# Kernel optimization log

Hardware: AMD Instinct MI355X
Metric: run time of the kernel (lower is better)

## Reference

```python
import jax, jax.numpy as jnp
import numpy as np

D_MODEL = 1024
N_HEADS = 16


def setup_inputs() -> dict:
    key = jax.random.key(0)
    ks = jax.random.split(key, 11)
    B, S = 4, 2048
    sc = 1.0 / np.sqrt(D_MODEL)
    inp = {
        "Q": jax.random.normal(ks[0], (B, S, D_MODEL), jnp.float32),
        "K": jax.random.normal(ks[1], (B, S, D_MODEL), jnp.float32),
        "V": jax.random.normal(ks[2], (B, S, D_MODEL), jnp.float32),
        "Wq": jax.random.normal(ks[3], (D_MODEL, D_MODEL), jnp.float32) * sc,
        "bq": jnp.zeros((D_MODEL,), jnp.float32),
        "Wk": jax.random.normal(ks[4], (D_MODEL, D_MODEL), jnp.float32) * sc,
        "bk": jnp.zeros((D_MODEL,), jnp.float32),
        "Wv": jax.random.normal(ks[5], (D_MODEL, D_MODEL), jnp.float32) * sc,
        "bv": jnp.zeros((D_MODEL,), jnp.float32),
        "Wo": jax.random.normal(ks[6], (D_MODEL, D_MODEL), jnp.float32) * sc,
        "bo": jnp.zeros((D_MODEL,), jnp.float32),
    }
    return inp


def reference(Q, K, V, Wq, bq, Wk, bk, Wv, bv, Wo, bo):
    B, Sq, d_model = Q.shape
    h = N_HEADS
    d_k = d_model // h

    def split_heads(x, W, b):
        y = x @ W.T + b                     # (B, S, d_model)
        return y.reshape(B, x.shape[1], h, d_k).transpose(0, 2, 1, 3)  # (B,h,S,d_k)

    q = split_heads(Q, Wq, bq)
    k = split_heads(K, Wk, bk)
    v = split_heads(V, Wv, bv)

    scores = jnp.einsum("bhqd,bhkd->bhqk", q, k) / jnp.sqrt(jnp.asarray(d_k, q.dtype))
    attn = jax.nn.softmax(scores.astype(jnp.float32), axis=-1).astype(q.dtype)
    out = jnp.einsum("bhqk,bhkd->bhqd", attn, v)  # (B,h,Sq,d_k)
    out = out.transpose(0, 2, 1, 3).reshape(B, Sq, d_model)
    return out @ Wo.T + bo
```

## Files before the change

kernel.cpp:

```cpp
#include <hip/hip_runtime.h>
#include <stdint.h>

#define DM    1024
#define NH    16
#define DKH   64
#define SEQ   2048
#define NB    4
#define MROWS (NB * SEQ)

typedef __attribute__((ext_vector_type(4))) float f32x4;
typedef __attribute__((ext_vector_type(8))) short s16x8;
typedef __attribute__((ext_vector_type(4))) unsigned short u16x4;
typedef __attribute__((ext_vector_type(8))) unsigned short u16x8;

__device__ __forceinline__ unsigned short f2bf(float f) {
  union { float f; uint32_t u; } v; v.f = f;
  uint32_t r = v.u + 0x7fffu + ((v.u >> 16) & 1u);
  return (unsigned short)(r >> 16);
}

__device__ __forceinline__ void gload16(const void* g, void* l) {
  __builtin_amdgcn_global_load_lds(
      (__attribute__((address_space(1))) void*)(uintptr_t)g,
      (__attribute__((address_space(3))) void*)(uint32_t)(uintptr_t)l,
      16, 0, 0);
}

__device__ __forceinline__ float exp2fast(float x) {
#if __has_builtin(__builtin_amdgcn_exp2f)
  return __builtin_amdgcn_exp2f(x);
#else
  return exp2f(x);
#endif
}

__device__ __forceinline__ unsigned int cvtpk(float a, float b) {
  unsigned int r;
  asm("v_cvt_pk_bf16_f32 %0, %1, %2" : "=v"(r) : "v"(a), "v"(b));
  return r;
}

__device__ __forceinline__ float bperm(float v, int srclane) {
  union { float f; int i; } u; u.f = v;
  u.i = __builtin_amdgcn_ds_bpermute(srclane << 2, u.i);
  return u.f;
}

__device__ __forceinline__ void cvt8(const float* in, unsigned short* out, int i) {
  const f32x4* p = (const f32x4*)(in + i);
  f32x4 a = p[0], b = p[1];
  u16x8 r;
#pragma unroll
  for (int j = 0; j < 4; ++j) { r[j] = f2bf(a[j]); r[4 + j] = f2bf(b[j]); }
  *(u16x8*)(out + i) = r;
}

__global__ __launch_bounds__(256) void cvt3_kernel(const float* __restrict__ a,
                                                   const float* __restrict__ b,
                                                   const float* __restrict__ c,
                                                   unsigned short* __restrict__ oa,
                                                   unsigned short* __restrict__ ob,
                                                   unsigned short* __restrict__ oc) {
  const int seg = blockIdx.x >> 12;
  const int blk = blockIdx.x & 4095;
  const float* in = (seg == 0) ? a : (seg == 1) ? b : c;
  unsigned short* out = (seg == 0) ? oa : (seg == 1) ? ob : oc;
  cvt8(in, out, (blk * 256 + threadIdx.x) * 8);
}

__global__ __launch_bounds__(256) void cvt4_kernel(const float* __restrict__ a,
                                                   const float* __restrict__ b,
                                                   const float* __restrict__ c,
                                                   const float* __restrict__ d,
                                                   unsigned short* __restrict__ oa,
                                                   unsigned short* __restrict__ ob,
                                                   unsigned short* __restrict__ oc,
                                                   unsigned short* __restrict__ od) {
  const int seg = blockIdx.x >> 9;
  const int blk = blockIdx.x & 511;
  const float* in = (seg == 0) ? a : (seg == 1) ? b : (seg == 2) ? c : d;
  unsigned short* out = (seg == 0) ? oa : (seg == 1) ? ob : (seg == 2) ? oc : od;
  cvt8(in, out, (blk * 256 + threadIdx.x) * 8);
}

template <int MODE>
__global__ __launch_bounds__(256) void gemm_bt(const unsigned short* __restrict__ A,
                                               const unsigned short* __restrict__ Bw,
                                               const float* __restrict__ bias,
                                               void* __restrict__ out,
                                               float oscale) {
  __shared__ char smem[65536];

  int bid = (int)(blockIdx.y * 8 + blockIdx.x);
  bid = (bid & 7) * 64 + (bid >> 3);
  const int tcol = (bid & 7) * 128;
  const int trow = (bid >> 3) * 128;

  const int lane = threadIdx.x & 63;
  const int w    = threadIdx.x >> 6;
  const int wm = w >> 1, wn = w & 1;
  const int l15 = lane & 15, l4 = lane >> 4;

  f32x4 acc[4][4] = {};

  auto stage = [&](int buf, int k0) {
    char* As = smem + buf * 32768;
    char* Bs = As + 16384;
#pragma unroll
    for (int i = 0; i < 4; ++i) {
      const int row = i * 32 + w * 8 + (lane >> 3);
      const int sc  = ((lane & 7) ^ (row & 7)) << 3;
      gload16(A  + (size_t)(trow + row) * DM + k0 + sc, As + i * 4096 + w * 1024);
      gload16(Bw + (size_t)(tcol + row) * DM + k0 + sc, Bs + i * 4096 + w * 1024);
    }
  };

  stage(0, 0);
  __syncthreads();
  int cur = 0;

  for (int k0 = 0; k0 < DM; k0 += 64) {
    if (k0 + 64 < DM) stage(cur ^ 1, k0 + 64);
    char* As = smem + cur * 32768;
    char* Bs = As + 16384;

#pragma unroll
    for (int ks = 0; ks < 2; ++ks) {
      s16x8 af[4], bf[4];
#pragma unroll
      for (int x = 0; x < 4; ++x) {
        const int ra = wm * 64 + x * 16 + l15;
        const int rb = wn * 64 + x * 16 + l15;
        const int kb = ks * 4 + l4;
        af[x] = *(const s16x8*)(As + ra * 128 + ((kb ^ (ra & 7)) << 4));
        bf[x] = *(const s16x8*)(Bs + rb * 128 + ((kb ^ (rb & 7)) << 4));
      }
#pragma unroll
      for (int mi = 0; mi < 4; ++mi)
#pragma unroll
        for (int ni = 0; ni < 4; ++ni)
          acc[mi][ni] = __builtin_amdgcn_mfma_f32_16x16x32_bf16(af[mi], bf[ni], acc[mi][ni], 0, 0, 0);
    }
    __syncthreads();
    cur ^= 1;
  }

#pragma unroll
  for (int ni = 0; ni < 4; ++ni) {
    const int n  = tcol + wn * 64 + ni * 16 + l15;
    const float bv = bias[n];
#pragma unroll
    for (int mi = 0; mi < 4; ++mi) {
      const int m0 = trow + wm * 64 + mi * 16 + l4 * 4;
      if (MODE == 2) {
        float* o = (float*)out;
#pragma unroll
        for (int j = 0; j < 4; ++j)
          o[(size_t)(m0 + j) * DM + n] = acc[mi][ni][j] + bv;
      } else if (MODE == 0) {
        unsigned short* o = (unsigned short*)out;
        const int bb = m0 >> 11, h = n >> 6, dk = n & 63;
#pragma unroll
        for (int j = 0; j < 4; ++j) {
          const int s = (m0 + j) & 2047;
          o[(((size_t)bb * NH + h) * SEQ + s) * DKH + dk] = f2bf((acc[mi][ni][j] + bv) * oscale);
        }
      } else {
        unsigned short* o = (unsigned short*)out;
        const int bb = m0 >> 11, h = n >> 6, dk = n & 63, s = m0 & 2047;
        const int u = s & 31;
        const int s2 = (s & ~31) | ((u & 12) << 1) | ((u & 16) >> 2);
        u16x4 pk;
#pragma unroll
        for (int j = 0; j < 4; ++j) pk[j] = f2bf(acc[mi][ni][j] + bv);
        *(u16x4*)(o + (((size_t)bb * NH + h) * DKH + dk) * SEQ + s2) = pk;
      }
    }
  }
}

__global__ __launch_bounds__(256, 2) void attn_kernel(const unsigned short* __restrict__ qh,
                                                      const unsigned short* __restrict__ kh,
                                                      const unsigned short* __restrict__ vth,
                                                      unsigned short* __restrict__ ao) {
  __shared__ char smem[32768];

  int bid = (int)blockIdx.x;
  bid = (bid & 7) * 64 + (bid >> 3);
  const int bh = bid >> 3;
  const int q0 = (bid & 7) * 256;

  const int lane = threadIdx.x & 63;
  const int w    = threadIdx.x >> 6;
  const int l15 = lane & 15, l4 = lane >> 4;

  const int qrow = q0 + w * 64;
  const unsigned short* qbase = qh + ((size_t)bh * SEQ + qrow) * DKH;

  s16x8 qf[4][2];
#pragma unroll
  for (int ni = 0; ni < 4; ++ni)
#pragma unroll
    for (int ks = 0; ks < 2; ++ks)
      qf[ni][ks] = *(const s16x8*)(qbase + (ni * 16 + l15) * DKH + ks * 32 + l4 * 8);

  int koff[2][4], voff[2][4];
#pragma unroll
  for (int ks = 0; ks < 2; ++ks)
#pragma unroll
    for (int mi = 0; mi < 4; ++mi) {
      const int r = mi * 16 + l15;
      koff[ks][mi] = r * 128 + (((ks * 4 + l4) ^ (r & 7)) << 4);
    }
#pragma unroll
  for (int m = 0; m < 2; ++m)
#pragma unroll
    for (int nd = 0; nd < 4; ++nd) {
      const int r = nd * 16 + l15;
      voff[m][nd] = r * 128 + (((m * 4 + l4) ^ (r & 7)) << 4);
    }

  f32x4 o[4][4] = {};
  f32x4 lsum[4] = {};

  s16x8 onesB = (s16x8)0;
  if (l15 == 0) {
#pragma unroll
    for (int j = 0; j < 8; ++j) onesB[j] = (short)0x3F80;
  }

  const unsigned short* kbase = kh  + (size_t)bh * SEQ * DKH;
  const unsigned short* vbase = vth + (size_t)bh * DKH * SEQ;

  auto stageK = [&](int buf, int kv0) {
    char* Ks = smem + buf * 8192;
#pragma unroll
    for (int i = 0; i < 2; ++i) {
      const int row = i * 32 + w * 8 + (lane >> 3);
      const int sc  = ((lane & 7) ^ (row & 7)) << 3;
      gload16(kbase + (size_t)(kv0 + row) * DKH + sc, Ks + i * 4096 + w * 1024);
    }
  };
  auto stageV = [&](int buf, int kv0) {
    char* Vs = smem + 16384 + buf * 8192;
#pragma unroll
    for (int i = 0; i < 2; ++i) {
      const int row = i * 32 + w * 8 + (lane >> 3);
      const int sc  = ((lane & 7) ^ (row & 7)) << 3;
      gload16(vbase + (size_t)row * SEQ + kv0 + sc, Vs + i * 4096 + w * 1024);
    }
  };

  f32x4 sa[4][4];

  auto qkt = [&](const char* Ks) {
#pragma unroll
    for (int mi = 0; mi < 4; ++mi)
#pragma unroll
      for (int ni = 0; ni < 4; ++ni) sa[mi][ni] = (f32x4)0.f;
    __builtin_amdgcn_s_setprio(1);
#pragma unroll
    for (int ks = 0; ks < 2; ++ks) {
      s16x8 kf[4];
#pragma unroll
      for (int mi = 0; mi < 4; ++mi) kf[mi] = *(const s16x8*)(Ks + koff[ks][mi]);
#pragma unroll
      for (int mi = 0; mi < 4; ++mi)
#pragma unroll
        for (int ni = 0; ni < 4; ++ni)
          sa[mi][ni] = __builtin_amdgcn_mfma_f32_16x16x32_bf16(kf[mi], qf[ni][ks], sa[mi][ni], 0, 0, 0);
    }
    __builtin_amdgcn_s_setprio(0);
  };

  auto smpv = [&](const char* Vs) {
#pragma unroll
    for (int mi = 0; mi < 4; ++mi)
#pragma unroll
      for (int ni = 0; ni < 4; ++ni)
#pragma unroll
        for (int j = 0; j < 4; ++j)
          sa[mi][ni][j] = exp2fast(sa[mi][ni][j]);

    __builtin_amdgcn_s_setprio(1);
#pragma unroll
    for (int m = 0; m < 2; ++m) {
      s16x8 pa[4];
#pragma unroll
      for (int ni = 0; ni < 4; ++ni) {
        union { unsigned int u[4]; s16x8 v; } pu;
        pu.u[0] = cvtpk(sa[2 * m][ni][0],     sa[2 * m][ni][1]);
        pu.u[1] = cvtpk(sa[2 * m][ni][2],     sa[2 * m][ni][3]);
        pu.u[2] = cvtpk(sa[2 * m + 1][ni][0], sa[2 * m + 1][ni][1]);
        pu.u[3] = cvtpk(sa[2 * m + 1][ni][2], sa[2 * m + 1][ni][3]);
        pa[ni] = pu.v;
      }
#pragma unroll
      for (int ni = 0; ni < 4; ++ni)
        lsum[ni] = __builtin_amdgcn_mfma_f32_16x16x32_bf16(pa[ni], onesB, lsum[ni], 0, 0, 0);
#pragma unroll
      for (int nd = 0; nd < 4; ++nd) {
        const s16x8 vbf = *(const s16x8*)(Vs + voff[m][nd]);
#pragma unroll
        for (int ni = 0; ni < 4; ++ni)
          o[ni][nd] = __builtin_amdgcn_mfma_f32_16x16x32_bf16(pa[ni], vbf, o[ni][nd], 0, 0, 0);
      }
    }
    __builtin_amdgcn_s_setprio(0);
  };

  stageK(0, 0); stageV(0, 0);
  __syncthreads();

  for (int t = 0; t < 32; t += 2) {
    const int kv0 = t * 64;
    stageK(1, kv0 + 64); stageV(1, kv0 + 64);
    qkt(smem);
    smpv(smem + 16384);
    __syncthreads();
    if (t + 2 < 32) { stageK(0, kv0 + 128); stageV(0, kv0 + 128); }
    qkt(smem + 8192);
    smpv(smem + 16384 + 8192);
    __syncthreads();
  }

  const int bb = bh >> 4, h = bh & 15;
#pragma unroll
  for (int ni = 0; ni < 4; ++ni) {
#pragma unroll
    for (int j = 0; j < 4; ++j) {
      const float inv = 1.0f / bperm(lsum[ni][j], lane & 48);
      const int s = qrow + ni * 16 + l4 * 4 + j;
#pragma unroll
      for (int nd = 0; nd < 4; ++nd) {
        const int col = h * 64 + nd * 16 + l15;
        ao[((size_t)bb * SEQ + s) * DM + col] = f2bf(o[ni][nd][j] * inv);
      }
    }
  }
}

extern "C" void kernel_launch(void* const* d_in, const int* in_sizes, int n_in,
                              void* d_out, int out_size, void* d_ws, size_t ws_size,
                              hipStream_t stream) {
  const float* Q  = (const float*)d_in[0];
  const float* K  = (const float*)d_in[1];
  const float* V  = (const float*)d_in[2];
  const float* Wq = (const float*)d_in[3];
  const float* bq = (const float*)d_in[4];
  const float* Wk = (const float*)d_in[5];
  const float* bk = (const float*)d_in[6];
  const float* Wv = (const float*)d_in[7];
  const float* bv = (const float*)d_in[8];
  const float* Wo = (const float*)d_in[9];
  const float* bo = (const float*)d_in[10];
  float* out = (float*)d_out;

  char* ws = (char*)d_ws;
  const size_t MB = 1024 * 1024;
  unsigned short* Qb  = (unsigned short*)(ws + 0 * MB);
  unsigned short* Kb  = (unsigned short*)(ws + 16 * MB);
  unsigned short* Vb  = (unsigned short*)(ws + 32 * MB);
  unsigned short* Wqb = (unsigned short*)(ws + 48 * MB);
  unsigned short* Wkb = (unsigned short*)(ws + 50 * MB);
  unsigned short* Wvb = (unsigned short*)(ws + 52 * MB);
  unsigned short* Wob = (unsigned short*)(ws + 54 * MB);
  unsigned short* qhd = (unsigned short*)(ws + 56 * MB);
  unsigned short* khd = (unsigned short*)(ws + 72 * MB);
  unsigned short* vtd = (unsigned short*)(ws + 88 * MB);
  unsigned short* aod = (unsigned short*)(ws + 104 * MB);

  const float QSCALE = 0.18033688011112042f;

  cvt3_kernel<<<dim3(3 * 4096), 256, 0, stream>>>(Q, K, V, Qb, Kb, Vb);
  cvt4_kernel<<<dim3(4 * 512), 256, 0, stream>>>(Wq, Wk, Wv, Wo, Wqb, Wkb, Wvb, Wob);

  dim3 gg(DM / 128, MROWS / 128);
  gemm_bt<0><<<gg, 256, 0, stream>>>(Qb, Wqb, bq, qhd, QSCALE);
  gemm_bt<0><<<gg, 256, 0, stream>>>(Kb, Wkb, bk, khd, 1.0f);
  gemm_bt<1><<<gg, 256, 0, stream>>>(Vb, Wvb, bv, vtd, 1.0f);

  attn_kernel<<<dim3(512), 256, 0, stream>>>(qhd, khd, vtd, aod);

  gemm_bt<2><<<gg, 256, 0, stream>>>(aod, Wob, bo, out, 1.0f);
}
```

Baseline: 168.8 us.

## Fuse fp32-to-bf16 activation conversion into projection GEMM A-tile loading

Drops the separate Q/K/V conversion kernel. The QKV projection GEMMs now read fp32 activations into registers, convert them to bf16 with packed cvt, and write them into LDS with the same swizzle, overlapping the next tile's loads with compute. This removes a full fp32 read plus bf16 write and re-read of three 32MB activation tensors. In exchange each GEMM reads twice the A bytes, and register pressure rises from holding the prefetched fp32 tile.

Measured after the change: 164.4 us. 1.03x faster.

```diff
diff --git a/kernel.cpp b/kernel.cpp
--- a/kernel.cpp
+++ b/kernel.cpp
@@ -53,19 +53,6 @@
 #pragma unroll
   for (int j = 0; j < 4; ++j) { r[j] = f2bf(a[j]); r[4 + j] = f2bf(b[j]); }
   *(u16x8*)(out + i) = r;
-}
-
-__global__ __launch_bounds__(256) void cvt3_kernel(const float* __restrict__ a,
-                                                   const float* __restrict__ b,
-                                                   const float* __restrict__ c,
-                                                   unsigned short* __restrict__ oa,
-                                                   unsigned short* __restrict__ ob,
-                                                   unsigned short* __restrict__ oc) {
-  const int seg = blockIdx.x >> 12;
-  const int blk = blockIdx.x & 4095;
-  const float* in = (seg == 0) ? a : (seg == 1) ? b : c;
-  unsigned short* out = (seg == 0) ? oa : (seg == 1) ? ob : oc;
-  cvt8(in, out, (blk * 256 + threadIdx.x) * 8);
 }
 
 __global__ __launch_bounds__(256) void cvt4_kernel(const float* __restrict__ a,
@@ -83,8 +70,8 @@
   cvt8(in, out, (blk * 256 + threadIdx.x) * 8);
 }
 
-template <int MODE>
-__global__ __launch_bounds__(256) void gemm_bt(const unsigned short* __restrict__ A,
+template <int MODE, int AFP32>
+__global__ __launch_bounds__(256) void gemm_bt(const void* __restrict__ Ap,
                                                const unsigned short* __restrict__ Bw,
                                                const float* __restrict__ bias,
                                                void* __restrict__ out,
@@ -101,29 +88,51 @@
   const int wm = w >> 1, wn = w & 1;
   const int l15 = lane & 15, l4 = lane >> 4;
 
+  const float* Af = (const float*)Ap;
+  const unsigned short* Ah = (const unsigned short*)Ap;
+
+  const int srow = w * 8 + (lane >> 3);
+  const int sc   = ((lane & 7) ^ (lane >> 3)) * 8;
+  const int ldst = (lane & 7) * 16;
+
   f32x4 acc[4][4] = {};
-
-  auto stage = [&](int buf, int k0) {
+  f32x4 areg[4][2];
+
+  auto aload = [&](int k0) {
+#pragma unroll
+    for (int i = 0; i < 4; ++i) {
+      const float* p = Af + (size_t)(trow + i * 32 + srow) * DM + k0 + sc;
+      areg[i][0] = *(const f32x4*)p;
+      areg[i][1] = *(const f32x4*)(p + 4);
+    }
+  };
+  auto awrite = [&](int buf) {
+    char* As = smem + buf * 32768;
+#pragma unroll
+    for (int i = 0; i < 4; ++i) {
+      union { unsigned int u[4]; s16x8 v; } pu;
+      pu.u[0] = cvtpk(areg[i][0][0], areg[i][0][1]);
+      pu.u[1] = cvtpk(areg[i][0][2], areg[i][0][3]);
+      pu.u[2] = cvtpk(areg[i][1][0], areg[i][1][1]);
+      pu.u[3] = cvtpk(areg[i][1][2], areg[i][1][3]);
+      *(s16x8*)(As + (i * 32 + srow) * 128 + ldst) = pu.v;
+    }
+  };
+  auto astage = [&](int buf, int k0) {
+    char* As = smem + buf * 32768;
+#pragma unroll
+    for (int i = 0; i < 4; ++i)
+      gload16(Ah + (size_t)(trow + i * 32 + srow) * DM + k0 + sc, As + i * 4096 + w * 1024);
+  };
+  auto bstage = [&](int buf, int k0) {
+    char* Bs = smem + buf * 32768 + 16384;
+#pragma unroll
+    for (int i = 0; i < 4; ++i)
+      gload16(Bw + (size_t)(tcol + i * 32 + srow) * DM + k0 + sc, Bs + i * 4096 + w * 1024);
+  };
+  auto compute = [&](int buf) {
     char* As = smem + buf * 32768;
     char* Bs = As + 16384;
-#pragma unroll
-    for (int i = 0; i < 4; ++i) {
-      const int row = i * 32 + w * 8 + (lane >> 3);
-      const int sc  = ((lane & 7) ^ (row & 7)) << 3;
-      gload16(A  + (size_t)(trow + row) * DM + k0 + sc, As + i * 4096 + w * 1024);
-      gload16(Bw + (size_t)(tcol + row) * DM + k0 + sc, Bs + i * 4096 + w * 1024);
-    }
-  };
-
-  stage(0, 0);
-  __syncthreads();
-  int cur = 0;
-
-  for (int k0 = 0; k0 < DM; k0 += 64) {
-    if (k0 + 64 < DM) stage(cur ^ 1, k0 + 64);
-    char* As = smem + cur * 32768;
-    char* Bs = As + 16384;
-
 #pragma unroll
     for (int ks = 0; ks < 2; ++ks) {
       s16x8 af[4], bf[4];
@@ -141,6 +150,22 @@
         for (int ni = 0; ni < 4; ++ni)
           acc[mi][ni] = __builtin_amdgcn_mfma_f32_16x16x32_bf16(af[mi], bf[ni], acc[mi][ni], 0, 0, 0);
     }
+  };
+
+  if (AFP32) aload(0); else astage(0, 0);
+  bstage(0, 0);
+  if (AFP32) awrite(0);
+  __syncthreads();
+  int cur = 0;
+
+  for (int k0 = 0; k0 < DM; k0 += 64) {
+    const bool more = (k0 + 64 < DM);
+    if (more) {
+      if (AFP32) aload(k0 + 64); else astage(cur ^ 1, k0 + 64);
+      bstage(cur ^ 1, k0 + 64);
+    }
+    compute(cur);
+    if (more && AFP32) awrite(cur ^ 1);
     __syncthreads();
     cur ^= 1;
   }
@@ -358,29 +383,25 @@
 
   char* ws = (char*)d_ws;
   const size_t MB = 1024 * 1024;
-  unsigned short* Qb  = (unsigned short*)(ws + 0 * MB);
-  unsigned short* Kb  = (unsigned short*)(ws + 16 * MB);
-  unsigned short* Vb  = (unsigned short*)(ws + 32 * MB);
-  unsigned short* Wqb = (unsigned short*)(ws + 48 * MB);
-  unsigned short* Wkb = (unsigned short*)(ws + 50 * MB);
-  unsigned short* Wvb = (unsigned short*)(ws + 52 * MB);
-  unsigned short* Wob = (unsigned short*)(ws + 54 * MB);
-  unsigned short* qhd = (unsigned short*)(ws + 56 * MB);
-  unsigned short* khd = (unsigned short*)(ws + 72 * MB);
-  unsigned short* vtd = (unsigned short*)(ws + 88 * MB);
-  unsigned short* aod = (unsigned short*)(ws + 104 * MB);
+  unsigned short* Wqb = (unsigned short*)(ws + 0 * MB);
+  unsigned short* Wkb = (unsigned short*)(ws + 2 * MB);
+  unsigned short* Wvb = (unsigned short*)(ws + 4 * MB);
+  unsigned short* Wob = (unsigned short*)(ws + 6 * MB);
+  unsigned short* qhd = (unsigned short*)(ws + 8 * MB);
+  unsigned short* khd = (unsigned short*)(ws + 24 * MB);
+  unsigned short* vtd = (unsigned short*)(ws + 40 * MB);
+  unsigned short* aod = (unsigned short*)(ws + 56 * MB);
 
   const float QSCALE = 0.18033688011112042f;
 
-  cvt3_kernel<<<dim3(3 * 4096), 256, 0, stream>>>(Q, K, V, Qb, Kb, Vb);
   cvt4_kernel<<<dim3(4 * 512), 256, 0, stream>>>(Wq, Wk, Wv, Wo, Wqb, Wkb, Wvb, Wob);
 
   dim3 gg(DM / 128, MROWS / 128);
-  gemm_bt<0><<<gg, 256, 0, stream>>>(Qb, Wqb, bq, qhd, QSCALE);
-  gemm_bt<0><<<gg, 256, 0, stream>>>(Kb, Wkb, bk, khd, 1.0f);
-  gemm_bt<1><<<gg, 256, 0, stream>>>(Vb, Wvb, bv, vtd, 1.0f);
+  gemm_bt<0, 1><<<gg, 256, 0, stream>>>(Q, Wqb, bq, qhd, QSCALE);
+  gemm_bt<0, 1><<<gg, 256, 0, stream>>>(K, Wkb, bk, khd, 1.0f);
+  gemm_bt<1, 1><<<gg, 256, 0, stream>>>(V, Wvb, bv, vtd, 1.0f);
 
   attn_kernel<<<dim3(512), 256, 0, stream>>>(qhd, khd, vtd, aod);
 
-  gemm_bt<2><<<gg, 256, 0, stream>>>(aod, Wob, bo, out, 1.0f);
-}
+  gemm_bt<2, 0><<<gg, 256, 0, stream>>>(aod, Wob, bo, out, 1.0f);
+}
```
